# Kernel tuning notes

Measured on AMD Instinct MI355X. Metric: run time of the kernel, lower is better.

## Reference

```python
import jax, jax.numpy as jnp
import numpy as np

H = 2048        # hidden_size
E = 32          # n_routed_experts
I = 1024        # moe_intermediate_size
TOPK = 6        # num_experts_per_tok
NGROUP = 8      # n_group
TOPKG = 4       # topk_group
SHARED_I = 1024 # moe_intermediate_size * n_shared_experts
SCALE = 2.5     # routed_scaling_factor
T = 1024        # num_tokens


def setup_inputs() -> dict:
    key = jax.random.key(0)
    ks = jax.random.split(key, 7)
    s = 0.02
    return {
        "hidden_states": jax.random.normal(ks[0], (T, H), jnp.float32),
        "gate_w": jax.random.normal(ks[1], (H, E), jnp.float32) * s,
        "e_bias": jax.random.normal(ks[2], (E,), jnp.float32) * s,
        "w_gate_up": jax.random.normal(ks[3], (E, H, 2 * I), jnp.float32) * s,
        "w_down": jax.random.normal(ks[4], (E, I, H), jnp.float32) * s,
        "shared_gate_up": jax.random.normal(ks[5], (H, 2 * SHARED_I), jnp.float32) * s,
        "shared_down": jax.random.normal(ks[6], (SHARED_I, H), jnp.float32) * s,
    }


def _silu_and_mul(gu):
    g, u = jnp.split(gu, 2, axis=-1)
    return jax.nn.silu(g) * u


def _grouped_topk(logits, bias):
    # DeepSeek-V3 style 'noaux_tc' grouped top-k with sigmoid scoring.
    Tn, En = logits.shape
    scores = jax.nn.sigmoid(logits)                 # [T, E]
    scores_choice = scores + bias                   # biased scores used for selection only
    gsize = En // NGROUP
    grp = scores_choice.reshape(Tn, NGROUP, gsize)
    # group score = sum of top-2 biased scores within each group
    group_scores = jnp.sum(jax.lax.top_k(grp, 2)[0], axis=-1)   # [T, G]
    _, gidx = jax.lax.top_k(group_scores, TOPKG)                # [T, topk_group]
    gmask = jnp.sum(jax.nn.one_hot(gidx, NGROUP, dtype=scores.dtype), axis=1)  # [T, G]
    emask = jnp.repeat(gmask, gsize, axis=1)                    # [T, E]
    masked = jnp.where(emask > 0, scores_choice, -jnp.inf)
    _, topk_ids = jax.lax.top_k(masked, TOPK)                   # [T, top_k]
    # weights come from the UNbiased scores, then renormalized (norm_topk_prob=True)
    topk_w = jnp.take_along_axis(scores, topk_ids, axis=1)
    topk_w = topk_w / jnp.sum(topk_w, axis=-1, keepdims=True)
    return topk_w, topk_ids


def _moe_forward(hidden_states, gate_w, e_bias, w_gate_up, w_down,
                 shared_gate_up, shared_down):
    Tn, _ = hidden_states.shape
    # shared expert MLP (reduce_results=False path, fp32 -> no 1/scale correction)
    shared = _silu_and_mul(hidden_states @ shared_gate_up) @ shared_down
    # router
    logits = hidden_states @ gate_w
    topk_w, topk_ids = _grouped_topk(logits, e_bias)
    # sparse combine weights [T, E] (zero except top-k entries)
    combine = jnp.zeros((Tn, E), dtype=hidden_states.dtype)
    combine = combine.at[jnp.arange(Tn)[:, None], topk_ids].add(topk_w)
    # scan over experts, accumulating weighted expert-MLP outputs
    def body(acc, p):
        wgu, wd, w_e = p  # [H,2I], [I,H], [T]
        y = _silu_and_mul(hidden_states @ wgu) @ wd
        return acc + w_e[:, None] * y, None
    out, _ = jax.lax.scan(body, jnp.zeros_like(hidden_states),
                          (w_gate_up, w_down, combine.T))
    return out * SCALE + shared


def reference(hidden_states, gate_w, e_bias, w_gate_up, w_down,
              shared_gate_up, shared_down):
    return _moe_forward(hidden_states, gate_w, e_bias, w_gate_up, w_down,
                        shared_gate_up, shared_down)
```

## Files before the change

### kernel.cpp

```cpp
#include <hip/hip_runtime.h>
#include <stdint.h>

#define TT 1024
#define HH 2048
#define NE 32
#define II 1024
#define NTOPK 6
#define SCALEF 2.5f

typedef __attribute__((ext_vector_type(4))) float f32x4;
typedef __attribute__((ext_vector_type(8))) __bf16 bf16x8;

#define GLD16(g, l)                                                                         \
  __builtin_amdgcn_global_load_lds((const __attribute__((address_space(1))) void*)(g),      \
                                   (__attribute__((address_space(3))) void*)(l), 16, 0, 0)

__device__ __forceinline__ unsigned bf16rne(float f) {
    unsigned u = __builtin_bit_cast(unsigned, f);
    return (u + 0x7FFFu + ((u >> 16) & 1u)) >> 16;
}
__device__ __forceinline__ unsigned pack2(float lo, float hi) {
    return bf16rne(lo) | (bf16rne(hi) << 16);
}

__global__ void init_convert(const float* __restrict__ x, unsigned short* __restrict__ xb,
                             int* __restrict__ cnt, int* __restrict__ tlist,
                             float* __restrict__ twgt) {
    int gid = blockIdx.x * 256 + threadIdx.x;
    const float4* x4 = (const float4*)x;
    float4 v = x4[gid];
    uint2 o;
    o.x = pack2(v.x, v.y);
    o.y = pack2(v.z, v.w);
    ((uint2*)xb)[gid] = o;
    if (gid < TT) {
        tlist[(NE << 10) + gid] = gid;
        twgt[(NE << 10) + gid] = 1.0f;
    }
    if (gid == 0) cnt[NE] = TT;
}

__global__ void router_kernel(const float* __restrict__ x, const float* __restrict__ gw,
                              const float* __restrict__ bias, int* __restrict__ cnt,
                              int* __restrict__ tlist, float* __restrict__ twgt) {
    int t = blockIdx.x;
    int lane = threadIdx.x;
    int e = lane & 31, h = lane >> 5;
    const float* xr = x + (size_t)t * HH;
    float acc = 0.f;
    #pragma unroll 4
    for (int k = h; k < HH; k += 2)
        acc += xr[k] * gw[k * NE + e];
    acc += __shfl_down(acc, 32);

    __shared__ float sc[NE], sb[NE];
    if (lane < NE) {
        float s = 1.f / (1.f + expf(-acc));
        sc[e] = s;
        sb[e] = s + bias[e];
    }
    __syncthreads();
    if (lane == 0) {
        float gs[8];
        for (int g = 0; g < 8; g++) {
            float m1 = -1e30f, m2 = -1e30f;
            for (int j = 0; j < 4; j++) {
                float v = sb[g * 4 + j];
                if (v > m1) { m2 = m1; m1 = v; }
                else if (v > m2) { m2 = v; }
            }
            gs[g] = m1 + m2;
        }
        unsigned gmask = 0;
        for (int r = 0; r < 4; r++) {
            float best = -1e30f; int bi = 0;
            for (int g = 0; g < 8; g++)
                if (!((gmask >> g) & 1) && gs[g] > best) { best = gs[g]; bi = g; }
            gmask |= 1u << bi;
        }
        int ids[NTOPK]; float wsv[NTOPK]; float sum = 0.f;
        unsigned sel = 0;
        for (int r = 0; r < NTOPK; r++) {
            float best = -1e30f; int bi = 0;
            for (int ee = 0; ee < NE; ee++) {
                if (!((gmask >> (ee >> 2)) & 1)) continue;
                if ((sel >> ee) & 1) continue;
                if (sb[ee] > best) { best = sb[ee]; bi = ee; }
            }
            sel |= 1u << bi;
            ids[r] = bi; wsv[r] = sc[bi]; sum += sc[bi];
        }
        float inv = SCALEF / sum;
        for (int r = 0; r < NTOPK; r++) {
            int ee = ids[r];
            int slot = atomicAdd(&cnt[ee], 1);
            tlist[(ee << 10) + slot] = t;
            twgt[(ee << 10) + slot] = wsv[r] * inv;
        }
    }
}

__global__ __launch_bounds__(256, 2)
void gu_gemm(const unsigned short* __restrict__ xb,
             const float* __restrict__ wgu, const float* __restrict__ shgu,
             const int* __restrict__ tlist, const float* __restrict__ twgt,
             const int* __restrict__ cnt, unsigned short* __restrict__ act) {
    int e = blockIdx.z;
    int count = cnt[e];
    int m0 = blockIdx.y * 128;
    if (m0 >= count) return;
    int n0 = blockIdx.x * 64;
    const float* wb = (e < NE) ? (wgu + (size_t)e * HH * (2 * II)) : shgu;
    const int* tl = tlist + (e << 10);

    __shared__ __align__(16) unsigned short xs[128 * 32];
    __shared__ __align__(16) unsigned short wg[64 * 40];
    __shared__ __align__(16) unsigned short wu[64 * 40];

    int tid = threadIdx.x;
    int lane = tid & 63, wv = tid >> 6;
    int q = lane >> 4, c = lane & 15;

    int arow = wv * 16 + (lane >> 2);
    int akc = (lane & 3) * 8;
    int tok0 = (m0 + arow < count) ? tl[m0 + arow] : 0;
    int tok1 = (m0 + arow + 64 < count) ? tl[m0 + arow + 64] : 0;
    const unsigned short* ag0 = xb + (size_t)tok0 * HH + akc;
    const unsigned short* ag1 = xb + (size_t)tok1 * HH + akc;
    unsigned short* al0 = xs + (wv * 16) * 32;
    unsigned short* al1 = xs + (64 + wv * 16) * 32;

    int kp = tid & 15, ig = tid >> 4;
    int n4 = ig * 4;
    const float* wpbase = wb + (size_t)(kp * 2) * (2 * II) + n0 + n4;
    unsigned* wgd = (unsigned*)wg;
    unsigned* wud = (unsigned*)wu;
    int di = n4 * 20 + kp;

    f32x4 accg[2][4] = {};
    f32x4 accu[2][4] = {};

    for (int k0 = 0; k0 < HH; k0 += 32) {
        GLD16(ag0 + k0, al0);
        GLD16(ag1 + k0, al1);
        const float* wp = wpbase + (size_t)k0 * (2 * II);
        float4 g0 = *(const float4*)(wp);
        float4 g1 = *(const float4*)(wp + 2 * II);
        float4 u0 = *(const float4*)(wp + II);
        float4 u1 = *(const float4*)(wp + 2 * II + II);
        wgd[di]      = pack2(g0.x, g1.x);
        wgd[di + 20] = pack2(g0.y, g1.y);
        wgd[di + 40] = pack2(g0.z, g1.z);
        wgd[di + 60] = pack2(g0.w, g1.w);
        wud[di]      = pack2(u0.x, u1.x);
        wud[di + 20] = pack2(u0.y, u1.y);
        wud[di + 40] = pack2(u0.z, u1.z);
        wud[di + 60] = pack2(u0.w, u1.w);
        __syncthreads();
        bf16x8 a0 = *(const bf16x8*)(xs + (wv * 32 + c) * 32 + q * 8);
        bf16x8 a1 = *(const bf16x8*)(xs + (wv * 32 + 16 + c) * 32 + q * 8);
        #pragma unroll
        for (int tn = 0; tn < 4; tn++) {
            bf16x8 bg = *(const bf16x8*)(wg + (tn * 16 + c) * 40 + q * 8);
            bf16x8 bu = *(const bf16x8*)(wu + (tn * 16 + c) * 40 + q * 8);
            accg[0][tn] = __builtin_amdgcn_mfma_f32_16x16x32_bf16(a0, bg, accg[0][tn], 0, 0, 0);
            accg[1][tn] = __builtin_amdgcn_mfma_f32_16x16x32_bf16(a1, bg, accg[1][tn], 0, 0, 0);
            accu[0][tn] = __builtin_amdgcn_mfma_f32_16x16x32_bf16(a0, bu, accu[0][tn], 0, 0, 0);
            accu[1][tn] = __builtin_amdgcn_mfma_f32_16x16x32_bf16(a1, bu, accu[1][tn], 0, 0, 0);
        }
        __syncthreads();
    }

    const float* twp = twgt + (e << 10);
    #pragma unroll
    for (int tm = 0; tm < 2; tm++) {
        int mlb = wv * 32 + tm * 16 + q * 4;
        #pragma unroll
        for (int r = 0; r < 4; r++) {
            int m = m0 + mlb + r;
            if (m < count) {
                float w = twp[m];
                size_t rowbase = ((size_t)(e << 10) + m) * II + n0;
                #pragma unroll
                for (int tn = 0; tn < 4; tn++) {
                    float g = accg[tm][tn][r];
                    float u = accu[tm][tn][r];
                    float a = (g / (1.f + __expf(-g))) * u * w;
                    act[rowbase + tn * 16 + c] = (unsigned short)bf16rne(a);
                }
            }
        }
    }
}

__global__ __launch_bounds__(256, 2)
void down_gemm(const unsigned short* __restrict__ act,
               const float* __restrict__ wd, const float* __restrict__ shd,
               const int* __restrict__ tlist, const int* __restrict__ cnt,
               float* __restrict__ out) {
    int e = blockIdx.z;
    int count = cnt[e];
    int m0 = blockIdx.y * 128;
    if (m0 >= count) return;
    int n0 = blockIdx.x * 128;
    const float* wb = (e < NE) ? (wd + (size_t)e * II * HH) : shd;
    const int* tl = tlist + (e << 10);

    __shared__ __align__(16) unsigned short as_[128 * 32];
    __shared__ __align__(16) unsigned short bs[128 * 40];

    int tid = threadIdx.x;
    int lane = tid & 63, wv = tid >> 6;
    int q = lane >> 4, c = lane & 15;

    const unsigned short* ag =
        act + ((size_t)(e << 10) + m0 + wv * 16 + (lane >> 2)) * II + (lane & 3) * 8;
    unsigned short* al0 = as_ + (wv * 16) * 32;
    unsigned short* al1 = as_ + (64 + wv * 16) * 32;

    int kp = tid & 15, ig = tid >> 4;
    int n4 = ig * 4;
    const float* wpbase = wb + (size_t)(kp * 2) * HH + n0 + n4;
    unsigned* bd = (unsigned*)bs;
    int di0 = n4 * 20 + kp;
    int di1 = (n4 + 64) * 20 + kp;

    f32x4 acc[2][8] = {};

    for (int k0 = 0; k0 < II; k0 += 32) {
        GLD16(ag + k0, al0);
        GLD16(ag + (size_t)64 * II + k0, al1);
        const float* wp = wpbase + (size_t)k0 * HH;
        float4 x0 = *(const float4*)(wp);
        float4 x1 = *(const float4*)(wp + HH);
        float4 y0 = *(const float4*)(wp + 64);
        float4 y1 = *(const float4*)(wp + HH + 64);
        bd[di0]      = pack2(x0.x, x1.x);
        bd[di0 + 20] = pack2(x0.y, x1.y);
        bd[di0 + 40] = pack2(x0.z, x1.z);
        bd[di0 + 60] = pack2(x0.w, x1.w);
        bd[di1]      = pack2(y0.x, y1.x);
        bd[di1 + 20] = pack2(y0.y, y1.y);
        bd[di1 + 40] = pack2(y0.z, y1.z);
        bd[di1 + 60] = pack2(y0.w, y1.w);
        __syncthreads();
        bf16x8 a0 = *(const bf16x8*)(as_ + (wv * 32 + c) * 32 + q * 8);
        bf16x8 a1 = *(const bf16x8*)(as_ + (wv * 32 + 16 + c) * 32 + q * 8);
        #pragma unroll
        for (int tn = 0; tn < 8; tn++) {
            bf16x8 b = *(const bf16x8*)(bs + (tn * 16 + c) * 40 + q * 8);
            acc[0][tn] = __builtin_amdgcn_mfma_f32_16x16x32_bf16(a0, b, acc[0][tn], 0, 0, 0);
            acc[1][tn] = __builtin_amdgcn_mfma_f32_16x16x32_bf16(a1, b, acc[1][tn], 0, 0, 0);
        }
        __syncthreads();
    }

    #pragma unroll
    for (int tm = 0; tm < 2; tm++) {
        int mlb = wv * 32 + tm * 16 + q * 4;
        #pragma unroll
        for (int r = 0; r < 4; r++) {
            int m = m0 + mlb + r;
            if (m < count) {
                int tok = tl[m];
                float* op = out + (size_t)tok * HH + n0 + c;
                #pragma unroll
                for (int tn = 0; tn < 8; tn++)
                    unsafeAtomicAdd(op + tn * 16, acc[tm][tn][r]);
            }
        }
    }
}

extern "C" void kernel_launch(void* const* d_in, const int* in_sizes, int n_in,
                              void* d_out, int out_size, void* d_ws, size_t ws_size,
                              hipStream_t stream) {
    const float* x    = (const float*)d_in[0];
    const float* gw   = (const float*)d_in[1];
    const float* bias = (const float*)d_in[2];
    const float* wgu  = (const float*)d_in[3];
    const float* wd   = (const float*)d_in[4];
    const float* shgu = (const float*)d_in[5];
    const float* shd  = (const float*)d_in[6];
    float* out = (float*)d_out;

    char* ws = (char*)d_ws;
    int*   cnt   = (int*)ws;
    int*   tlist = (int*)(ws + 256);
    float* twgt  = (float*)(ws + 256 + 33 * 1024 * 4);
    unsigned short* xb  = (unsigned short*)(ws + 256 + 2 * 33 * 1024 * 4);
    unsigned short* act = (unsigned short*)((char*)xb + (size_t)TT * HH * 2);

    hipMemsetAsync(cnt, 0, 256, stream);
    hipMemsetAsync(out, 0, (size_t)out_size * sizeof(float), stream);
    init_convert<<<dim3((TT * HH / 4) / 256), 256, 0, stream>>>(x, xb, cnt, tlist, twgt);
    router_kernel<<<dim3(TT), 64, 0, stream>>>(x, gw, bias, cnt, tlist, twgt);
    gu_gemm<<<dim3(II / 64, 8, NE + 1), 256, 0, stream>>>(xb, wgu, shgu, tlist, twgt, cnt, act);
    down_gemm<<<dim3(HH / 128, 8, NE + 1), 256, 0, stream>>>(act, wd, shd, tlist, cnt, out);
}
```

Measured before the change: 1.235 ms.

## Double-buffer LDS tiles and prefetch next K-slice in both MoE GEMMs

Result: no change. 1.228 ms (-0.5%).

```diff
diff --git a/kernel.cpp b/kernel.cpp
--- a/kernel.cpp
+++ b/kernel.cpp
@@ -10,6 +10,7 @@
 
 typedef __attribute__((ext_vector_type(4))) float f32x4;
 typedef __attribute__((ext_vector_type(8))) __bf16 bf16x8;
+typedef unsigned short us;
 
 #define GLD16(g, l)                                                                         \
   __builtin_amdgcn_global_load_lds((const __attribute__((address_space(1))) void*)(g),      \
@@ -23,7 +24,7 @@
     return bf16rne(lo) | (bf16rne(hi) << 16);
 }
 
-__global__ void init_convert(const float* __restrict__ x, unsigned short* __restrict__ xb,
+__global__ void init_convert(const float* __restrict__ x, us* __restrict__ xb,
                              int* __restrict__ cnt, int* __restrict__ tlist,
                              float* __restrict__ twgt) {
     int gid = blockIdx.x * 256 + threadIdx.x;
@@ -100,11 +101,11 @@
     }
 }
 
-__global__ __launch_bounds__(256, 2)
-void gu_gemm(const unsigned short* __restrict__ xb,
+__global__ __launch_bounds__(256, 3)
+void gu_gemm(const us* __restrict__ xb,
              const float* __restrict__ wgu, const float* __restrict__ shgu,
              const int* __restrict__ tlist, const float* __restrict__ twgt,
-             const int* __restrict__ cnt, unsigned short* __restrict__ act) {
+             const int* __restrict__ cnt, us* __restrict__ act) {
     int e = blockIdx.z;
     int count = cnt[e];
     int m0 = blockIdx.y * 128;
@@ -113,9 +114,9 @@
     const float* wb = (e < NE) ? (wgu + (size_t)e * HH * (2 * II)) : shgu;
     const int* tl = tlist + (e << 10);
 
-    __shared__ __align__(16) unsigned short xs[128 * 32];
-    __shared__ __align__(16) unsigned short wg[64 * 40];
-    __shared__ __align__(16) unsigned short wu[64 * 40];
+    __shared__ __align__(16) us xs[2][128 * 32];
+    __shared__ __align__(16) us wg[2][64 * 40];
+    __shared__ __align__(16) us wu[2][64 * 40];
 
     int tid = threadIdx.x;
     int lane = tid & 63, wv = tid >> 6;
@@ -125,29 +126,30 @@
     int akc = (lane & 3) * 8;
     int tok0 = (m0 + arow < count) ? tl[m0 + arow] : 0;
     int tok1 = (m0 + arow + 64 < count) ? tl[m0 + arow + 64] : 0;
-    const unsigned short* ag0 = xb + (size_t)tok0 * HH + akc;
-    const unsigned short* ag1 = xb + (size_t)tok1 * HH + akc;
-    unsigned short* al0 = xs + (wv * 16) * 32;
-    unsigned short* al1 = xs + (64 + wv * 16) * 32;
+    const us* ag0 = xb + (size_t)tok0 * HH + akc;
+    const us* ag1 = xb + (size_t)tok1 * HH + akc;
+    int aoff0 = (wv * 16) * 32;
+    int aoff1 = (64 + wv * 16) * 32;
 
     int kp = tid & 15, ig = tid >> 4;
     int n4 = ig * 4;
     const float* wpbase = wb + (size_t)(kp * 2) * (2 * II) + n0 + n4;
-    unsigned* wgd = (unsigned*)wg;
-    unsigned* wud = (unsigned*)wu;
     int di = n4 * 20 + kp;
 
     f32x4 accg[2][4] = {};
     f32x4 accu[2][4] = {};
 
+    GLD16(ag0, xs[0] + aoff0);
+    GLD16(ag1, xs[0] + aoff1);
+    float4 g0 = *(const float4*)(wpbase);
+    float4 g1 = *(const float4*)(wpbase + 2 * II);
+    float4 u0 = *(const float4*)(wpbase + II);
+    float4 u1 = *(const float4*)(wpbase + 2 * II + II);
+
+    int cur = 0;
     for (int k0 = 0; k0 < HH; k0 += 32) {
-        GLD16(ag0 + k0, al0);
-        GLD16(ag1 + k0, al1);
-        const float* wp = wpbase + (size_t)k0 * (2 * II);
-        float4 g0 = *(const float4*)(wp);
-        float4 g1 = *(const float4*)(wp + 2 * II);
-        float4 u0 = *(const float4*)(wp + II);
-        float4 u1 = *(const float4*)(wp + 2 * II + II);
+        unsigned* wgd = (unsigned*)wg[cur];
+        unsigned* wud = (unsigned*)wu[cur];
         wgd[di]      = pack2(g0.x, g1.x);
         wgd[di + 20] = pack2(g0.y, g1.y);
         wgd[di + 40] = pack2(g0.z, g1.z);
@@ -157,18 +159,33 @@
         wud[di + 40] = pack2(u0.z, u1.z);
         wud[di + 60] = pack2(u0.w, u1.w);
         __syncthreads();
-        bf16x8 a0 = *(const bf16x8*)(xs + (wv * 32 + c) * 32 + q * 8);
-        bf16x8 a1 = *(const bf16x8*)(xs + (wv * 32 + 16 + c) * 32 + q * 8);
+
+        int k1 = k0 + 32;
+        if (k1 < HH) {
+            GLD16(ag0 + k1, xs[cur ^ 1] + aoff0);
+            GLD16(ag1 + k1, xs[cur ^ 1] + aoff1);
+            const float* wp = wpbase + (size_t)k1 * (2 * II);
+            g0 = *(const float4*)(wp);
+            g1 = *(const float4*)(wp + 2 * II);
+            u0 = *(const float4*)(wp + II);
+            u1 = *(const float4*)(wp + 2 * II + II);
+        }
+
+        const us* xsc = xs[cur];
+        const us* wgc = wg[cur];
+        const us* wuc = wu[cur];
+        bf16x8 a0 = *(const bf16x8*)(xsc + (wv * 32 + c) * 32 + q * 8);
+        bf16x8 a1 = *(const bf16x8*)(xsc + (wv * 32 + 16 + c) * 32 + q * 8);
         #pragma unroll
         for (int tn = 0; tn < 4; tn++) {
-            bf16x8 bg = *(const bf16x8*)(wg + (tn * 16 + c) * 40 + q * 8);
-            bf16x8 bu = *(const bf16x8*)(wu + (tn * 16 + c) * 40 + q * 8);
+            bf16x8 bg = *(const bf16x8*)(wgc + (tn * 16 + c) * 40 + q * 8);
+            bf16x8 bu = *(const bf16x8*)(wuc + (tn * 16 + c) * 40 + q * 8);
             accg[0][tn] = __builtin_amdgcn_mfma_f32_16x16x32_bf16(a0, bg, accg[0][tn], 0, 0, 0);
             accg[1][tn] = __builtin_amdgcn_mfma_f32_16x16x32_bf16(a1, bg, accg[1][tn], 0, 0, 0);
             accu[0][tn] = __builtin_amdgcn_mfma_f32_16x16x32_bf16(a0, bu, accu[0][tn], 0, 0, 0);
             accu[1][tn] = __builtin_amdgcn_mfma_f32_16x16x32_bf16(a1, bu, accu[1][tn], 0, 0, 0);
         }
-        __syncthreads();
+        cur ^= 1;
     }
 
     const float* twp = twgt + (e << 10);
@@ -186,15 +203,15 @@
                     float g = accg[tm][tn][r];
                     float u = accu[tm][tn][r];
                     float a = (g / (1.f + __expf(-g))) * u * w;
-                    act[rowbase + tn * 16 + c] = (unsigned short)bf16rne(a);
+                    act[rowbase + tn * 16 + c] = (us)bf16rne(a);
                 }
             }
         }
     }
 }
 
-__global__ __launch_bounds__(256, 2)
-void down_gemm(const unsigned short* __restrict__ act,
+__global__ __launch_bounds__(256, 3)
+void down_gemm(const us* __restrict__ act,
                const float* __restrict__ wd, const float* __restrict__ shd,
                const int* __restrict__ tlist, const int* __restrict__ cnt,
                float* __restrict__ out) {
@@ -206,35 +223,36 @@
     const float* wb = (e < NE) ? (wd + (size_t)e * II * HH) : shd;
     const int* tl = tlist + (e << 10);
 
-    __shared__ __align__(16) unsigned short as_[128 * 32];
-    __shared__ __align__(16) unsigned short bs[128 * 40];
+    __shared__ __align__(16) us as_[2][128 * 32];
+    __shared__ __align__(16) us bs[2][128 * 40];
 
     int tid = threadIdx.x;
     int lane = tid & 63, wv = tid >> 6;
     int q = lane >> 4, c = lane & 15;
 
-    const unsigned short* ag =
+    const us* ag =
         act + ((size_t)(e << 10) + m0 + wv * 16 + (lane >> 2)) * II + (lane & 3) * 8;
-    unsigned short* al0 = as_ + (wv * 16) * 32;
-    unsigned short* al1 = as_ + (64 + wv * 16) * 32;
+    int aoff0 = (wv * 16) * 32;
+    int aoff1 = (64 + wv * 16) * 32;
 
     int kp = tid & 15, ig = tid >> 4;
     int n4 = ig * 4;
     const float* wpbase = wb + (size_t)(kp * 2) * HH + n0 + n4;
-    unsigned* bd = (unsigned*)bs;
     int di0 = n4 * 20 + kp;
     int di1 = (n4 + 64) * 20 + kp;
 
     f32x4 acc[2][8] = {};
 
+    GLD16(ag, as_[0] + aoff0);
+    GLD16(ag + (size_t)64 * II, as_[0] + aoff1);
+    float4 x0 = *(const float4*)(wpbase);
+    float4 x1 = *(const float4*)(wpbase + HH);
+    float4 y0 = *(const float4*)(wpbase + 64);
+    float4 y1 = *(const float4*)(wpbase + HH + 64);
+
+    int cur = 0;
     for (int k0 = 0; k0 < II; k0 += 32) {
-        GLD16(ag + k0, al0);
-        GLD16(ag + (size_t)64 * II + k0, al1);
-        const float* wp = wpbase + (size_t)k0 * HH;
-        float4 x0 = *(const float4*)(wp);
-        float4 x1 = *(const float4*)(wp + HH);
-        float4 y0 = *(const float4*)(wp + 64);
-        float4 y1 = *(const float4*)(wp + HH + 64);
+        unsigned* bd = (unsigned*)bs[cur];
         bd[di0]      = pack2(x0.x, x1.x);
         bd[di0 + 20] = pack2(x0.y, x1.y);
         bd[di0 + 40] = pack2(x0.z, x1.z);
@@ -244,15 +262,29 @@
         bd[di1 + 40] = pack2(y0.z, y1.z);
         bd[di1 + 60] = pack2(y0.w, y1.w);
         __syncthreads();
-        bf16x8 a0 = *(const bf16x8*)(as_ + (wv * 32 + c) * 32 + q * 8);
-        bf16x8 a1 = *(const bf16x8*)(as_ + (wv * 32 + 16 + c) * 32 + q * 8);
+
+        int k1 = k0 + 32;
+        if (k1 < II) {
+            GLD16(ag + k1, as_[cur ^ 1] + aoff0);
+            GLD16(ag + (size_t)64 * II + k1, as_[cur ^ 1] + aoff1);
+            const float* wp = wpbase + (size_t)k1 * HH;
+            x0 = *(const float4*)(wp);
+            x1 = *(const float4*)(wp + HH);
+            y0 = *(const float4*)(wp + 64);
+            y1 = *(const float4*)(wp + HH + 64);
+        }
+
+        const us* asc = as_[cur];
+        const us* bsc = bs[cur];
+        bf16x8 a0 = *(const bf16x8*)(asc + (wv * 32 + c) * 32 + q * 8);
+        bf16x8 a1 = *(const bf16x8*)(asc + (wv * 32 + 16 + c) * 32 + q * 8);
         #pragma unroll
         for (int tn = 0; tn < 8; tn++) {
-            bf16x8 b = *(const bf16x8*)(bs + (tn * 16 + c) * 40 + q * 8);
+            bf16x8 b = *(const bf16x8*)(bsc + (tn * 16 + c) * 40 + q * 8);
             acc[0][tn] = __builtin_amdgcn_mfma_f32_16x16x32_bf16(a0, b, acc[0][tn], 0, 0, 0);
             acc[1][tn] = __builtin_amdgcn_mfma_f32_16x16x32_bf16(a1, b, acc[1][tn], 0, 0, 0);
         }
-        __syncthreads();
+        cur ^= 1;
     }
 
     #pragma unroll
@@ -288,8 +320,8 @@
     int*   cnt   = (int*)ws;
     int*   tlist = (int*)(ws + 256);
     float* twgt  = (float*)(ws + 256 + 33 * 1024 * 4);
-    unsigned short* xb  = (unsigned short*)(ws + 256 + 2 * 33 * 1024 * 4);
-    unsigned short* act = (unsigned short*)((char*)xb + (size_t)TT * HH * 2);
+    us* xb  = (us*)(ws + 256 + 2 * 33 * 1024 * 4);
+    us* act = (us*)((char*)xb + (size_t)TT * HH * 2);
 
     hipMemsetAsync(cnt, 0, 256, stream);
     hipMemsetAsync(out, 0, (size_t)out_size * sizeof(float), stream);
```
